# Kernel tuning notes

Measured on AMD Instinct MI355X. Metric: run time of the kernel, lower is better.

Reference implementation:

```python
import jax, jax.numpy as jnp
import numpy as np

N, E, F, T, H = 100000, 3_200_000, 64, 12, 32


def _lin(k, fin, fout):
    s = 1.0 / np.sqrt(fin)
    k1, k2 = jax.random.split(k)
    W = jax.random.uniform(k1, (fin, fout), jnp.float32, -s, s)
    b = jax.random.uniform(k2, (fout,), jnp.float32, -s, s)
    return W, b


def _lstm_w(k, fin):
    s = 1.0 / np.sqrt(H)
    k1, k2, k3, k4 = jax.random.split(k, 4)
    return (jax.random.uniform(k1, (4 * H, fin), jnp.float32, -s, s),
            jax.random.uniform(k2, (4 * H, H), jnp.float32, -s, s),
            jax.random.uniform(k3, (4 * H,), jnp.float32, -s, s),
            jax.random.uniform(k4, (4 * H,), jnp.float32, -s, s))


def setup_inputs() -> dict:
    key = jax.random.key(0)
    ks = jax.random.split(key, 12)
    x = jax.random.normal(ks[0], (N, F), jnp.float32)
    edge_index = jax.random.randint(ks[1], (2, E), 0, N, dtype=jnp.int32)
    W_fp, b_fp = _lin(ks[2], F, 64)
    W_g1, b_g1 = _lin(ks[3], 64, 64)
    W_g2, b_g2 = _lin(ks[4], 64, 32)
    W_g3, b_g3 = _lin(ks[5], 32, 16)
    W_tp, b_tp = _lin(ks[6], 1, 16)
    Wih0, Whh0, bih0, bhh0 = _lstm_w(ks[7], 16)
    Wih1, Whh1, bih1, bhh1 = _lstm_w(ks[8], H)
    W_fc1, b_fc1 = _lin(ks[9], H, 16)
    W_fc2, b_fc2 = _lin(ks[10], 16, 1)
    return dict(x=x, edge_index=edge_index, W_fp=W_fp, b_fp=b_fp,
                W_g1=W_g1, b_g1=b_g1, W_g2=W_g2, b_g2=b_g2, W_g3=W_g3, b_g3=b_g3,
                W_tp=W_tp, b_tp=b_tp,
                Wih0=Wih0, Whh0=Whh0, bih0=bih0, bhh0=bhh0,
                Wih1=Wih1, Whh1=Whh1, bih1=bih1, bhh1=bhh1,
                W_fc1=W_fc1, b_fc1=b_fc1, W_fc2=W_fc2, b_fc2=b_fc2)


def reference(x, edge_index, W_fp, b_fp, W_g1, b_g1, W_g2, b_g2, W_g3, b_g3,
              W_tp, b_tp, Wih0, Whh0, bih0, bhh0, Wih1, Whh1, bih1, bhh1,
              W_fc1, b_fc1, W_fc2, b_fc2):
    n = x.shape[0]
    loops = jnp.arange(n, dtype=edge_index.dtype)
    src = jnp.concatenate([edge_index[0], loops])  # self-loops, PyG GCNConv default
    dst = jnp.concatenate([edge_index[1], loops])
    deg = jax.ops.segment_sum(jnp.ones_like(src, dtype=x.dtype), dst, num_segments=n)
    dis = deg ** -0.5  # deg >= 1 because of self-loops
    norm = dis[src] * dis[dst]  # [E+N]

    def gcn(h, W, b):
        h = h @ W  # transform then propagate (PyG order)
        agg = jax.ops.segment_sum(h[src] * norm[:, None], dst, num_segments=n)
        return agg + b

    h = jax.nn.relu(x @ W_fp + b_fp)
    h = jax.nn.relu(gcn(h, W_g1, b_g1))        # dropout inactive (eval mode)
    h = jax.nn.relu(gcn(h, W_g2, b_g2))
    h_gcn = jax.nn.relu(gcn(h, W_g3, b_g3))    # NOTE: overwritten in original forward (dead)

    # temporal branch: last T raw features -> [N, T, 1] -> proj to 16
    t = x[:, -T:].reshape(n, T, 1) @ W_tp + b_tp  # [N, T, 16]

    def step(carry, xt):
        h0, c0, h1, c1 = carry
        g = xt @ Wih0.T + h0 @ Whh0.T + (bih0 + bhh0)
        i, f, gg, o = jnp.split(g, 4, axis=-1)  # torch gate order i,f,g,o
        c0 = jax.nn.sigmoid(f) * c0 + jax.nn.sigmoid(i) * jnp.tanh(gg)
        h0 = jax.nn.sigmoid(o) * jnp.tanh(c0)
        g = h0 @ Wih1.T + h1 @ Whh1.T + (bih1 + bhh1)
        i, f, gg, o = jnp.split(g, 4, axis=-1)
        c1 = jax.nn.sigmoid(f) * c1 + jax.nn.sigmoid(i) * jnp.tanh(gg)
        h1 = jax.nn.sigmoid(o) * jnp.tanh(c1)
        return (h0, c0, h1, c1), None

    z = jnp.zeros((n, H), x.dtype)
    (h0, c0, h1, c1), _ = jax.lax.scan(step, (z, z, z, z), jnp.swapaxes(t, 0, 1))
    out = jax.nn.relu(h1 @ W_fc1 + b_fc1) @ W_fc2 + b_fc2  # [N, 1]
    return out
```

## Files before the change

kernel.cpp:

```cpp
#include <hip/hip_runtime.h>


#define TSTEPS 12
#define BS 512
#define NPB (BS / 4)

__device__ __forceinline__ float fsig(float x) {
    float e = __expf(-x);
    return __builtin_amdgcn_rcpf(1.0f + e);
}

__device__ __forceinline__ float ftanh(float x) {
    float ax = fabsf(x);
    float e = __expf(-2.0f * ax);
    float r = (1.0f - e) * __builtin_amdgcn_rcpf(1.0f + e);
    return x < 0.0f ? -r : r;
}

__global__ void precomp_kernel(const float* __restrict__ Wih0,
                               const float* __restrict__ Wtp,
                               const float* __restrict__ btp,
                               const float* __restrict__ bih0,
                               const float* __restrict__ bhh0,
                               const float* __restrict__ bih1,
                               const float* __restrict__ bhh1,
                               float* __restrict__ ws) {
    int r = threadIdx.x;
    if (r < 128) {
        float a = 0.0f, c = 0.0f;
#pragma unroll
        for (int k = 0; k < 16; ++k) {
            float w = Wih0[r * 16 + k];
            a += w * Wtp[k];
            c += w * btp[k];
        }
        ws[r]       = a;
        ws[128 + r] = c + bih0[r] + bhh0[r];
        ws[256 + r] = bih1[r] + bhh1[r];
    }
}

__device__ __forceinline__ float dot8(const float4 a0, const float4 a1,
                                      const float h[8]) {
    return a0.x*h[0] + a0.y*h[1] + a0.z*h[2] + a0.w*h[3]
         + a1.x*h[4] + a1.y*h[5] + a1.z*h[6] + a1.w*h[7];
}

__global__ __launch_bounds__(BS) void lstm_kernel(
    const float* __restrict__ x,
    const float* __restrict__ Whh0,
    const float* __restrict__ Wih1,
    const float* __restrict__ Whh1,
    const float* __restrict__ Wfc1,
    const float* __restrict__ bfc1,
    const float* __restrict__ Wfc2,
    const float* __restrict__ bfc2,
    const float* __restrict__ pre,
    float* __restrict__ out, int N)
{
    __shared__ __align__(16) float sW[12288];

    const int tid = threadIdx.x;
#pragma unroll
    for (int i = 0; i < 8; ++i) sW[i * BS + tid]        = Whh0[i * BS + tid];
#pragma unroll
    for (int i = 0; i < 8; ++i) sW[4096 + i * BS + tid] = Wih1[i * BS + tid];
#pragma unroll
    for (int i = 0; i < 8; ++i) sW[8192 + i * BS + tid] = Whh1[i * BS + tid];
    __syncthreads();

    const int s    = tid & 3;
    const int node = tid >> 2;
    const int so8  = s * 8;
    const int n  = blockIdx.x * NPB + node;
    const int nn = (n < N) ? n : (N > 0 ? N - 1 : 0);
    const float* xr = x + (size_t)nn * 64 + 52;

    float h0r[8], h1r[8], c0r[8], c1r[8], hn[8];
#pragma unroll
    for (int k = 0; k < 8; ++k) { h0r[k] = 0.0f; h1r[k] = 0.0f; c0r[k] = 0.0f; c1r[k] = 0.0f; }

#pragma unroll 1
    for (int t = 0; t < TSTEPS; ++t) {
        const float xval = xr[t];

#pragma unroll
        for (int jj = 0; jj < 8; ++jj) {
#pragma unroll 1
            for (int g = 0; g < 4; ++g) {
                const int j = g * 8 + jj;
                const float* wi = &sW[(j      ) * 32 + so8];
                const float* wf = &sW[(j +  32) * 32 + so8];
                const float* wg = &sW[(j +  64) * 32 + so8];
                const float* wo = &sW[(j +  96) * 32 + so8];
                float pi = dot8(((const float4*)wi)[0], ((const float4*)wi)[1], h0r);
                float pf = dot8(((const float4*)wf)[0], ((const float4*)wf)[1], h0r);
                float pg = dot8(((const float4*)wg)[0], ((const float4*)wg)[1], h0r);
                float po = dot8(((const float4*)wo)[0], ((const float4*)wo)[1], h0r);
                pi += __shfl_xor(pi, 1); pi += __shfl_xor(pi, 2);
                pf += __shfl_xor(pf, 1); pf += __shfl_xor(pf, 2);
                pg += __shfl_xor(pg, 1); pg += __shfl_xor(pg, 2);
                po += __shfl_xor(po, 1); po += __shfl_xor(po, 2);
                const float gi = pi + pre[128 + j] + xval * pre[j];
                const float gf = pf + pre[160 + j] + xval * pre[32 + j];
                const float gg = pg + pre[192 + j] + xval * pre[64 + j];
                const float go = po + pre[224 + j] + xval * pre[96 + j];
                const float cc = fsig(gf) * c0r[jj] + fsig(gi) * ftanh(gg);
                const float hh = fsig(go) * ftanh(cc);
                if (s == g) { c0r[jj] = cc; hn[jj] = hh; }
            }
        }
#pragma unroll
        for (int k = 0; k < 8; ++k) h0r[k] = hn[k];

#pragma unroll
        for (int jj = 0; jj < 8; ++jj) {
#pragma unroll 1
            for (int g = 0; g < 4; ++g) {
                const int j = g * 8 + jj;
                const float* ai = &sW[4096 + (j      ) * 32 + so8];
                const float* af = &sW[4096 + (j +  32) * 32 + so8];
                const float* ag = &sW[4096 + (j +  64) * 32 + so8];
                const float* ao = &sW[4096 + (j +  96) * 32 + so8];
                const float* bi = &sW[8192 + (j      ) * 32 + so8];
                const float* bf = &sW[8192 + (j +  32) * 32 + so8];
                const float* bg = &sW[8192 + (j +  64) * 32 + so8];
                const float* bo = &sW[8192 + (j +  96) * 32 + so8];
                float pi = dot8(((const float4*)ai)[0], ((const float4*)ai)[1], h0r)
                         + dot8(((const float4*)bi)[0], ((const float4*)bi)[1], h1r);
                float pf = dot8(((const float4*)af)[0], ((const float4*)af)[1], h0r)
                         + dot8(((const float4*)bf)[0], ((const float4*)bf)[1], h1r);
                float pg = dot8(((const float4*)ag)[0], ((const float4*)ag)[1], h0r)
                         + dot8(((const float4*)bg)[0], ((const float4*)bg)[1], h1r);
                float po = dot8(((const float4*)ao)[0], ((const float4*)ao)[1], h0r)
                         + dot8(((const float4*)bo)[0], ((const float4*)bo)[1], h1r);
                pi += __shfl_xor(pi, 1); pi += __shfl_xor(pi, 2);
                pf += __shfl_xor(pf, 1); pf += __shfl_xor(pf, 2);
                pg += __shfl_xor(pg, 1); pg += __shfl_xor(pg, 2);
                po += __shfl_xor(po, 1); po += __shfl_xor(po, 2);
                const float gi = pi + pre[256 + j];
                const float gf = pf + pre[288 + j];
                const float gg = pg + pre[320 + j];
                const float go = po + pre[352 + j];
                const float cc = fsig(gf) * c1r[jj] + fsig(gi) * ftanh(gg);
                const float hh = fsig(go) * ftanh(cc);
                if (s == g) { c1r[jj] = cc; hn[jj] = hh; }
            }
        }
#pragma unroll
        for (int k = 0; k < 8; ++k) h1r[k] = hn[k];
    }

    float am[16];
#pragma unroll
    for (int m = 0; m < 16; ++m) am[m] = 0.0f;
#pragma unroll 1
    for (int kk = 0; kk < 8; ++kk) {
        const float* row = Wfc1 + (size_t)(so8 + kk) * 16;
        const float4 r0 = ((const float4*)row)[0];
        const float4 r1 = ((const float4*)row)[1];
        const float4 r2 = ((const float4*)row)[2];
        const float4 r3 = ((const float4*)row)[3];
        const float hv = h1r[kk];
        am[ 0] += r0.x*hv; am[ 1] += r0.y*hv; am[ 2] += r0.z*hv; am[ 3] += r0.w*hv;
        am[ 4] += r1.x*hv; am[ 5] += r1.y*hv; am[ 6] += r1.z*hv; am[ 7] += r1.w*hv;
        am[ 8] += r2.x*hv; am[ 9] += r2.y*hv; am[10] += r2.z*hv; am[11] += r2.w*hv;
        am[12] += r3.x*hv; am[13] += r3.y*hv; am[14] += r3.z*hv; am[15] += r3.w*hv;
    }
    float acc = bfc2[0];
#pragma unroll
    for (int m = 0; m < 16; ++m) {
        float a = am[m];
        a += __shfl_xor(a, 1); a += __shfl_xor(a, 2);
        acc += fmaxf(a + bfc1[m], 0.0f) * Wfc2[m];
    }
    if (s == 0 && n < N) out[n] = acc;
}

extern "C" void kernel_launch(void* const* d_in, const int* in_sizes, int n_in,
                              void* d_out, int out_size, void* d_ws, size_t ws_size,
                              hipStream_t stream) {
    (void)n_in; (void)out_size; (void)ws_size;
    const float* x    = (const float*)d_in[0];
    const float* Wtp  = (const float*)d_in[10];
    const float* btp  = (const float*)d_in[11];
    const float* Wih0 = (const float*)d_in[12];
    const float* Whh0 = (const float*)d_in[13];
    const float* bih0 = (const float*)d_in[14];
    const float* bhh0 = (const float*)d_in[15];
    const float* Wih1 = (const float*)d_in[16];
    const float* Whh1 = (const float*)d_in[17];
    const float* bih1 = (const float*)d_in[18];
    const float* bhh1 = (const float*)d_in[19];
    const float* Wfc1 = (const float*)d_in[20];
    const float* bfc1 = (const float*)d_in[21];
    const float* Wfc2 = (const float*)d_in[22];
    const float* bfc2 = (const float*)d_in[23];

    float* out = (float*)d_out;
    float* pre = (float*)d_ws;

    const int N = in_sizes[0] / 64;

    precomp_kernel<<<1, 128, 0, stream>>>(Wih0, Wtp, btp, bih0, bhh0, bih1, bhh1, pre);
    lstm_kernel<<<(N + NPB - 1) / NPB, BS, 0, stream>>>(
        x, Whh0, Wih1, Whh1, Wfc1, bfc1, Wfc2, bfc2, pre, out, N);
}
```

Before: 1.458 ms.

## Use reduce-scatter across lane quad so each lane computes only its own gates

Replaces the per-gate allreduce, in which all four lanes computed every activation redundantly and kept one result, with a reduce-scatter (rs4). Each lane ends up with the full gate sums for its own hidden unit, so it evaluates the sigmoid and tanh activations once rather than four times. The shuffle count per group of four gate sums also drops. The precomputed bias and input-projection table is reordered so each lane loads its four gate constants with float4 reads. Sched barriers are added to control instruction ordering, at the cost of holding more partial sums in registers.

```diff
diff --git a/kernel.cpp b/kernel.cpp
--- a/kernel.cpp
+++ b/kernel.cpp
@@ -34,9 +34,11 @@
             a += w * Wtp[k];
             c += w * btp[k];
         }
-        ws[r]       = a;
-        ws[128 + r] = c + bih0[r] + bhh0[r];
-        ws[256 + r] = bih1[r] + bhh1[r];
+        const int g4 = r >> 5;
+        const int j  = r & 31;
+        ws[j * 8 + g4]       = a;
+        ws[j * 8 + 4 + g4]   = c + bih0[r] + bhh0[r];
+        ws[256 + j * 4 + g4] = bih1[r] + bhh1[r];
     }
 }
 
@@ -44,6 +46,19 @@
                                       const float h[8]) {
     return a0.x*h[0] + a0.y*h[1] + a0.z*h[2] + a0.w*h[3]
          + a1.x*h[4] + a1.y*h[5] + a1.z*h[6] + a1.w*h[7];
+}
+
+__device__ __forceinline__ float rs4(float v0, float v1, float v2, float v3,
+                                     bool hi2, bool hi1) {
+    float sa = hi2 ? v0 : v2;
+    float ka = hi2 ? v2 : v0;
+    float sb = hi2 ? v1 : v3;
+    float kb = hi2 ? v3 : v1;
+    float u0 = ka + __shfl_xor(sa, 2);
+    float u1 = kb + __shfl_xor(sb, 2);
+    float sc = hi1 ? u0 : u1;
+    float kc = hi1 ? u1 : u0;
+    return kc + __shfl_xor(sc, 1);
 }
 
 __global__ __launch_bounds__(BS) void lstm_kernel(
@@ -72,6 +87,8 @@
     const int s    = tid & 3;
     const int node = tid >> 2;
     const int so8  = s * 8;
+    const bool hi2 = (s & 2) != 0;
+    const bool hi1 = (s & 1) != 0;
     const int n  = blockIdx.x * NPB + node;
     const int nn = (n < N) ? n : (N > 0 ? N - 1 : 0);
     const float* xr = x + (size_t)nn * 64 + 52;
@@ -86,66 +103,80 @@
 
 #pragma unroll
         for (int jj = 0; jj < 8; ++jj) {
-#pragma unroll 1
+            const int jown = so8 + jj;
+            float pI[4], pF[4], pG[4], pO[4];
+#pragma unroll
             for (int g = 0; g < 4; ++g) {
                 const int j = g * 8 + jj;
                 const float* wi = &sW[(j      ) * 32 + so8];
                 const float* wf = &sW[(j +  32) * 32 + so8];
                 const float* wg = &sW[(j +  64) * 32 + so8];
                 const float* wo = &sW[(j +  96) * 32 + so8];
-                float pi = dot8(((const float4*)wi)[0], ((const float4*)wi)[1], h0r);
-                float pf = dot8(((const float4*)wf)[0], ((const float4*)wf)[1], h0r);
-                float pg = dot8(((const float4*)wg)[0], ((const float4*)wg)[1], h0r);
-                float po = dot8(((const float4*)wo)[0], ((const float4*)wo)[1], h0r);
-                pi += __shfl_xor(pi, 1); pi += __shfl_xor(pi, 2);
-                pf += __shfl_xor(pf, 1); pf += __shfl_xor(pf, 2);
-                pg += __shfl_xor(pg, 1); pg += __shfl_xor(pg, 2);
-                po += __shfl_xor(po, 1); po += __shfl_xor(po, 2);
-                const float gi = pi + pre[128 + j] + xval * pre[j];
-                const float gf = pf + pre[160 + j] + xval * pre[32 + j];
-                const float gg = pg + pre[192 + j] + xval * pre[64 + j];
-                const float go = po + pre[224 + j] + xval * pre[96 + j];
-                const float cc = fsig(gf) * c0r[jj] + fsig(gi) * ftanh(gg);
-                const float hh = fsig(go) * ftanh(cc);
-                if (s == g) { c0r[jj] = cc; hn[jj] = hh; }
+                pI[g] = dot8(((const float4*)wi)[0], ((const float4*)wi)[1], h0r);
+                pF[g] = dot8(((const float4*)wf)[0], ((const float4*)wf)[1], h0r);
+                pG[g] = dot8(((const float4*)wg)[0], ((const float4*)wg)[1], h0r);
+                pO[g] = dot8(((const float4*)wo)[0], ((const float4*)wo)[1], h0r);
+                __builtin_amdgcn_sched_barrier(0);
             }
+            const float SI = rs4(pI[0], pI[1], pI[2], pI[3], hi2, hi1);
+            const float SF = rs4(pF[0], pF[1], pF[2], pF[3], hi2, hi1);
+            const float SG = rs4(pG[0], pG[1], pG[2], pG[3], hi2, hi1);
+            const float SO = rs4(pO[0], pO[1], pO[2], pO[3], hi2, hi1);
+            const float4 pA = ((const float4*)pre)[jown * 2];
+            const float4 pC = ((const float4*)pre)[jown * 2 + 1];
+            const float gi = SI + pC.x + xval * pA.x;
+            const float gf = SF + pC.y + xval * pA.y;
+            const float gG = SG + pC.z + xval * pA.z;
+            const float go = SO + pC.w + xval * pA.w;
+            const float cc = fsig(gf) * c0r[jj] + fsig(gi) * ftanh(gG);
+            c0r[jj] = cc;
+            hn[jj]  = fsig(go) * ftanh(cc);
         }
 #pragma unroll
         for (int k = 0; k < 8; ++k) h0r[k] = hn[k];
 
 #pragma unroll
         for (int jj = 0; jj < 8; ++jj) {
-#pragma unroll 1
+            const int jown = so8 + jj;
+            float pI[4], pF[4], pG[4], pO[4];
+#pragma unroll
             for (int g = 0; g < 4; ++g) {
                 const int j = g * 8 + jj;
-                const float* ai = &sW[4096 + (j      ) * 32 + so8];
-                const float* af = &sW[4096 + (j +  32) * 32 + so8];
-                const float* ag = &sW[4096 + (j +  64) * 32 + so8];
-                const float* ao = &sW[4096 + (j +  96) * 32 + so8];
-                const float* bi = &sW[8192 + (j      ) * 32 + so8];
-                const float* bf = &sW[8192 + (j +  32) * 32 + so8];
-                const float* bg = &sW[8192 + (j +  64) * 32 + so8];
-                const float* bo = &sW[8192 + (j +  96) * 32 + so8];
-                float pi = dot8(((const float4*)ai)[0], ((const float4*)ai)[1], h0r)
-                         + dot8(((const float4*)bi)[0], ((const float4*)bi)[1], h1r);
-                float pf = dot8(((const float4*)af)[0], ((const float4*)af)[1], h0r)
-                         + dot8(((const float4*)bf)[0], ((const float4*)bf)[1], h1r);
-                float pg = dot8(((const float4*)ag)[0], ((const float4*)ag)[1], h0r)
-                         + dot8(((const float4*)bg)[0], ((const float4*)bg)[1], h1r);
-                float po = dot8(((const float4*)ao)[0], ((const float4*)ao)[1], h0r)
-                         + dot8(((const float4*)bo)[0], ((const float4*)bo)[1], h1r);
-                pi += __shfl_xor(pi, 1); pi += __shfl_xor(pi, 2);
-                pf += __shfl_xor(pf, 1); pf += __shfl_xor(pf, 2);
-                pg += __shfl_xor(pg, 1); pg += __shfl_xor(pg, 2);
-                po += __shfl_xor(po, 1); po += __shfl_xor(po, 2);
-                const float gi = pi + pre[256 + j];
-                const float gf = pf + pre[288 + j];
-                const float gg = pg + pre[320 + j];
-                const float go = po + pre[352 + j];
-                const float cc = fsig(gf) * c1r[jj] + fsig(gi) * ftanh(gg);
-                const float hh = fsig(go) * ftanh(cc);
-                if (s == g) { c1r[jj] = cc; hn[jj] = hh; }
+                {
+                    const float* ai = &sW[4096 + (j      ) * 32 + so8];
+                    const float* af = &sW[4096 + (j +  32) * 32 + so8];
+                    const float* ag = &sW[4096 + (j +  64) * 32 + so8];
+                    const float* ao = &sW[4096 + (j +  96) * 32 + so8];
+                    pI[g] = dot8(((const float4*)ai)[0], ((const float4*)ai)[1], h0r);
+                    pF[g] = dot8(((const float4*)af)[0], ((const float4*)af)[1], h0r);
+                    pG[g] = dot8(((const float4*)ag)[0], ((const float4*)ag)[1], h0r);
+                    pO[g] = dot8(((const float4*)ao)[0], ((const float4*)ao)[1], h0r);
+                }
+                __builtin_amdgcn_sched_barrier(0);
+                {
+                    const float* bi = &sW[8192 + (j      ) * 32 + so8];
+                    const float* bf = &sW[8192 + (j +  32) * 32 + so8];
+                    const float* bg = &sW[8192 + (j +  64) * 32 + so8];
+                    const float* bo = &sW[8192 + (j +  96) * 32 + so8];
+                    pI[g] += dot8(((const float4*)bi)[0], ((const float4*)bi)[1], h1r);
+                    pF[g] += dot8(((const float4*)bf)[0], ((const float4*)bf)[1], h1r);
+                    pG[g] += dot8(((const float4*)bg)[0], ((const float4*)bg)[1], h1r);
+                    pO[g] += dot8(((const float4*)bo)[0], ((const float4*)bo)[1], h1r);
+                }
+                __builtin_amdgcn_sched_barrier(0);
             }
+            const float SI = rs4(pI[0], pI[1], pI[2], pI[3], hi2, hi1);
+            const float SF = rs4(pF[0], pF[1], pF[2], pF[3], hi2, hi1);
+            const float SG = rs4(pG[0], pG[1], pG[2], pG[3], hi2, hi1);
+            const float SO = rs4(pO[0], pO[1], pO[2], pO[3], hi2, hi1);
+            const float4 pD = ((const float4*)(pre + 256))[jown];
+            const float gi = SI + pD.x;
+            const float gf = SF + pD.y;
+            const float gG = SG + pD.z;
+            const float go = SO + pD.w;
+            const float cc = fsig(gf) * c1r[jj] + fsig(gi) * ftanh(gG);
+            c1r[jj] = cc;
+            hn[jj]  = fsig(go) * ftanh(cc);
         }
 #pragma unroll
         for (int k = 0; k < 8; ++k) h1r[k] = hn[k];
```

Result: faster. 1.262 ms (-13.5%).
